# Performance work log

Hardware: AMD Instinct MI355X
Metric: run time of the kernel (lower is better)

Reference implementation:

```python
import jax, jax.numpy as jnp
import numpy as np
from jax import lax

# ---- module constants (match init_kwargs) ----
B, C, H, W = 8, 32, 128, 128
OUT = 32
RB = 1                      # refer_band
GB = (1, 1)                 # init_guard_band
GB_MAX = 3
PAD = GB[0] + RB            # replication pad on all 4 sides (=2)
KH = GB[0] + GB[1] + 2 * RB # kernel_size[0] = 4
KW = 4                      # kernel_size[1]
N = KH * KW                 # 16 ring sampling points
EPS = 1e-5


def _gen_prf():
    """Ring offsets (top,right,bottom,left blocks), matches _gen_prf_grid."""
    rb, gb = RB, GB
    h_prf = (rb + gb[0]) * 2 + 1
    w_prf = (rb + gb[1]) * 2 + 1
    xs = np.arange(-(rb + gb[0]), rb + gb[0] + 1)
    ys = np.arange(-(rb + gb[1]), rb + gb[1] + 1)
    X, Y = np.meshgrid(xs, ys, indexing='ij')
    def ring(A):
        t = A[0:rb, 0:w_prf - rb]
        r = A[0:h_prf - rb, w_prf - rb:w_prf]
        d = A[h_prf - rb:h_prf, rb:w_prf]
        l = A[rb:h_prf, 0:rb]
        return np.concatenate([t.ravel(), r.ravel(), d.ravel(), l.ravel()])
    return ring(X).astype(np.float32), ring(Y).astype(np.float32)

PRF_X, PRF_Y = _gen_prf()  # each (N,)


def _conv(x, w, b, pad, stride=(1, 1)):
    out = lax.conv_general_dilated(
        x, w, stride, [(pad[0], pad[0]), (pad[1], pad[1])],
        dimension_numbers=('NCHW', 'OIHW', 'NCHW'))
    return out + b[None, :, None, None]


def _bn(x, gamma, beta):
    # training-mode batchnorm (biased variance), matching torch default
    m = jnp.mean(x, (0, 2, 3), keepdims=True)
    v = jnp.var(x, (0, 2, 3), keepdims=True)
    return (x - m) * jax.lax.rsqrt(v + EPS) * gamma[None, :, None, None] + beta[None, :, None, None]


def _sample(x_flat, ix, iy, Wp, h, w):
    # x_flat: (B, C, Hp*Wp); ix, iy: (B, h, w, N) int -> (B, C, h, w, N)
    b = ix.shape[0]
    c = x_flat.shape[1]
    idx = (ix * Wp + iy).reshape(b, 1, -1)
    g = jnp.take_along_axis(x_flat, idx, axis=2)
    return g.reshape(b, c, h, w, N)


def _forward(x, w_vrt, b_vrt, g_vrt, be_vrt, w_hrz, b_hrz, g_hrz, be_hrz, w_pk, b_pk):
    b, c, h, w = x.shape
    x_pad = jnp.pad(x, ((0, 0), (0, 0), (PAD, PAD), (PAD, PAD)), mode='edge')
    Hp, Wp = x_pad.shape[2], x_pad.shape[3]
    x_flat = x_pad.reshape(b, c, Hp * Wp)

    # ---- BandEst: per-pixel guard-band widths in 4 directions (B,4,H,W) ----
    v = jax.nn.sigmoid(_bn(_conv(x, w_vrt, b_vrt, (GB_MAX, 0)), g_vrt, be_vrt)) * (GB_MAX - 1)
    hz = jax.nn.sigmoid(_bn(_conv(x, w_hrz, b_hrz, (0, GB_MAX)), g_hrz, be_hrz)) * (GB_MAX - 1)
    gb = jnp.concatenate([v, hz], axis=1)

    # ---- reference-cell sampling positions p = center + ring + learned move ----
    base_x = (jnp.arange(h, dtype=x.dtype) + PAD)[None, :, None, None]
    base_y = (jnp.arange(w, dtype=x.dtype) + PAD)[None, None, :, None]
    p_x = base_x + jnp.asarray(PRF_X)[None, None, None, :]  # (1,H,1,N)->bcast
    p_y = base_y + jnp.asarray(PRF_Y)[None, None, None, :]

    n4 = N // 4  # points per ring side (t,r,d,l ordering)
    def rep(g2):  # (B,H,W) -> (B,H,W,n4)
        return jnp.broadcast_to(g2[..., None], (b, h, w, n4))
    zeros = jnp.zeros((b, h, w, n4), x.dtype)
    move_x = jnp.concatenate([-rep(gb[:, 0]), zeros, rep(gb[:, 1]), zeros], -1)
    move_y = jnp.concatenate([zeros, rep(gb[:, 3]), zeros, -rep(gb[:, 2])], -1)
    p_x = p_x + move_x  # (B,H,W,N)
    p_y = p_y + move_y

    # ---- bilinear (two-corner) gather, mirrors torch q_lt/q_rb/g_lt/g_rb ----
    q_lt_x = jnp.floor(lax.stop_gradient(p_x))
    q_lt_y = jnp.floor(lax.stop_gradient(p_y))
    q_rb_x, q_rb_y = q_lt_x + 1, q_lt_y + 1
    q_lt_xi = jnp.clip(q_lt_x, 0, Hp - 1).astype(jnp.int32)
    q_lt_yi = jnp.clip(q_lt_y, 0, Wp - 1).astype(jnp.int32)
    q_rb_xi = jnp.clip(q_rb_x, 0, Hp - 1).astype(jnp.int32)
    q_rb_yi = jnp.clip(q_rb_y, 0, Wp - 1).astype(jnp.int32)
    p_x = jnp.clip(p_x, 0, Hp - 1)
    p_y = jnp.clip(p_y, 0, Wp - 1)

    g_lt = (1 + (q_lt_xi.astype(p_x.dtype) - p_x)) * (1 + (q_lt_yi.astype(p_y.dtype) - p_y))
    g_rb = (1 - (q_rb_xi.astype(p_x.dtype) - p_x)) * (1 - (q_rb_yi.astype(p_y.dtype) - p_y))

    x_q_lt = _sample(x_flat, q_lt_xi, q_lt_yi, Wp, h, w)  # (B,C,H,W,N)
    x_q_rb = _sample(x_flat, q_rb_xi, q_rb_yi, Wp, h, w)
    x_r = g_lt[:, None] * x_q_lt + g_rb[:, None] * x_q_rb

    # center value x_c equals x itself (center indices land in the interior)
    x_prf = x[:, :, :, :, None] - x_r  # (B,C,H,W,N)

    # ---- _reshape_x_prf: (B,C,H,W,N) -> (B,C,H*KH,W*KW) ----
    xk = x_prf.reshape(b, c, h, w, KH, KW).transpose(0, 1, 2, 4, 3, 5).reshape(b, c, h * KH, w * KW)

    # ---- peak conv: kernel = stride = (KH,KW), no padding ----
    return _conv(xk, w_pk, b_pk, (0, 0), stride=(KH, KW))


def setup_inputs() -> dict:
    key = jax.random.key(0)
    ks = jax.random.split(key, 8)
    s = 0.05
    return {
        'x': jax.random.normal(ks[0], (B, C, H, W), jnp.float32),
        'w_vrt': jax.random.normal(ks[1], (2, C, 2 * GB_MAX + 1, 1), jnp.float32) * s,
        'b_vrt': jax.random.normal(ks[2], (2,), jnp.float32) * s,
        'g_vrt': jnp.ones((2,), jnp.float32),
        'be_vrt': jnp.zeros((2,), jnp.float32),
        'w_hrz': jax.random.normal(ks[3], (2, C, 1, 2 * GB_MAX + 1), jnp.float32) * s,
        'b_hrz': jax.random.normal(ks[4], (2,), jnp.float32) * s,
        'g_hrz': jnp.ones((2,), jnp.float32),
        'be_hrz': jnp.zeros((2,), jnp.float32),
        'w_pk': jax.random.normal(ks[5], (OUT, C, KH, KW), jnp.float32) * s,
        'b_pk': jax.random.normal(ks[6], (OUT,), jnp.float32) * s,
    }


def reference(x, w_vrt, b_vrt, g_vrt, be_vrt, w_hrz, b_hrz, g_hrz, be_hrz, w_pk, b_pk):
    return _forward(x, w_vrt, b_vrt, g_vrt, be_vrt, w_hrz, b_hrz, g_hrz, be_hrz, w_pk, b_pk)
```

## Files before the change

kernel.cpp:

```cpp
#include <hip/hip_runtime.h>
#include <math.h>

#define BB 8
#define CCH 32
#define HH 128
#define WW 128
#define OUTC 32
#define NPIX (BB*HH*WW)
#define HWP 131

#define WS_XTB   0
#define WS_VO2   2097152
#define WS_HO2   (WS_VO2 + NPIX*2)
#define WS_PARTV (WS_HO2 + NPIX*2)
#define WS_PARTH (WS_PARTV + 2048*4)
#define WS_WKB   (WS_PARTH + 1024*4)

#define TILE_USH (12*40*5*8)

typedef __attribute__((ext_vector_type(8))) short short8;
typedef __attribute__((ext_vector_type(4))) float f32x4;

__device__ __forceinline__ unsigned short f2bf(float f) {
    unsigned u = __float_as_uint(f);
    unsigned r = (u + 0x7FFFu + ((u >> 16) & 1u)) >> 16;
    return (unsigned short)r;
}
__device__ __forceinline__ unsigned cvtpk(float lo, float hi) {
    unsigned r;
    asm("v_cvt_pk_bf16_f32 %0, %1, %2" : "=v"(r) : "v"(lo), "v"(hi));
    return r;
}
__device__ __forceinline__ float bflo(unsigned w) { return __uint_as_float(w << 16); }
__device__ __forceinline__ float bfhi(unsigned w) { return __uint_as_float(w & 0xFFFF0000u); }

__global__ __launch_bounds__(256) void k_fused1(const float* __restrict__ x,
        const float* __restrict__ w_vrt, const float* __restrict__ b_vrt,
        const float* __restrict__ w_hrz, const float* __restrict__ b_hrz,
        const float* __restrict__ w_pk, float* __restrict__ ws) {
    __shared__ unsigned sbuf[12288];
    int blk = blockIdx.x, t = threadIdx.x;
    if (blk < 256) {
        int jh = blk & 1, istr = (blk >> 1) & 15, b = blk >> 5;
        int i0 = istr * 8;
        int px = t & 63;
        int sub = __builtin_amdgcn_readfirstlane(t >> 6);
        int col = jh * 64 + px;
        unsigned* xp = sbuf;
        float* red_v = (float*)(sbuf + 8192);
        float vo[8][2];
        #pragma unroll
        for (int r = 0; r < 8; r++) { vo[r][0] = 0.f; vo[r][1] = 0.f; }
        float prev[8];
        for (int c8 = 0; c8 < 8; c8++) {
            int c = sub * 8 + c8;
            const float* basec = x + ((size_t)(b*CCH + c))*HH*WW;
            float xv[14];
            #pragma unroll
            for (int rr = 0; rr < 14; rr++) {
                int gr = i0 - 3 + rr;
                xv[rr] = ((unsigned)gr < (unsigned)HH) ? basec[(size_t)gr*WW + col] : 0.f;
            }
            #pragma unroll
            for (int r = 0; r < 8; r++) {
                #pragma unroll
                for (int k = 0; k < 7; k++) {
                    float wv0 = w_vrt[c*7 + k], wv1 = w_vrt[224 + c*7 + k];
                    vo[r][0] += wv0 * xv[r + k];
                    vo[r][1] += wv1 * xv[r + k];
                }
            }
            if ((c8 & 1) == 0) {
                #pragma unroll
                for (int r = 0; r < 8; r++) prev[r] = xv[3 + r];
            } else {
                #pragma unroll
                for (int r = 0; r < 8; r++)
                    xp[(r*64 + px)*16 + sub*4 + (c8 >> 1)] = cvtpk(prev[r], xv[3 + r]);
            }
        }
        #pragma unroll
        for (int r = 0; r < 8; r++) {
            red_v[((sub*64 + px)*8 + r)*2 + 0] = vo[r][0];
            red_v[((sub*64 + px)*8 + r)*2 + 1] = vo[r][1];
        }
        __syncthreads();
        float2* vo2 = (float2*)(ws + WS_VO2);
        #pragma unroll
        for (int h2 = 0; h2 < 2; h2++) {
            int r2 = sub * 2 + h2;
            float fv0 = red_v[((0*64 + px)*8 + r2)*2 + 0] + red_v[((1*64 + px)*8 + r2)*2 + 0]
                      + red_v[((2*64 + px)*8 + r2)*2 + 0] + red_v[((3*64 + px)*8 + r2)*2 + 0]
                      + b_vrt[0];
            float fv1 = red_v[((0*64 + px)*8 + r2)*2 + 1] + red_v[((1*64 + px)*8 + r2)*2 + 1]
                      + red_v[((2*64 + px)*8 + r2)*2 + 1] + red_v[((3*64 + px)*8 + r2)*2 + 1]
                      + b_vrt[1];
            int i = i0 + r2;
            vo2[(size_t)(b << 14) + i * WW + col] = make_float2(fv0, fv1);
            int cb = (b*HH + i)*2 + jh;
            float stv[4] = {fv0, fv1, fv0*fv0, fv1*fv1};
            #pragma unroll
            for (int u = 0; u < 4; u++) {
                float s = stv[u];
                for (int off = 32; off; off >>= 1) s += __shfl_down(s, off);
                if (px == 0) ws[WS_PARTV + cb*4 + u] = s;
            }
        }
        {
            uint4* xtb4 = (uint4*)(ws + WS_XTB);
            const uint4* xp4 = (const uint4*)xp;
            #pragma unroll
            for (int u = 0; u < 8; u++) {
                int e4 = u*256 + t;
                int rr = e4 >> 8, rem = e4 & 255, jj = rem >> 2, c4 = rem & 3;
                xtb4[(size_t)((b*HH + i0 + rr)*WW + jh*64 + jj)*4 + c4]
                    = xp4[(rr*64 + jj)*4 + c4];
            }
        }
    } else if (blk < 1280) {
        int e = blk - 256;
        int b = e >> 7, i = e & 127;
        int px2 = t & 63;
        int sub = __builtin_amdgcn_readfirstlane(t >> 6);
        float* red_h = (float*)sbuf;
        int cc[5]; bool mv[10];
        #pragma unroll
        for (int u = 0; u < 5; u++) {
            int c2 = 2*px2 - 4 + 2*u;
            cc[u] = min(max(c2, 0), WW - 2);
            mv[2*u]   = (unsigned)c2 < (unsigned)WW;
            mv[2*u+1] = (unsigned)(c2 + 1) < (unsigned)WW;
        }
        float h0A = 0.f, h1A = 0.f, h0B = 0.f, h1B = 0.f;
        for (int c8 = 0; c8 < 8; c8++) {
            int c = sub * 8 + c8;
            const float* rowb = x + ((size_t)(b*CCH + c)*HH + i)*WW;
            float lo[10];
            #pragma unroll
            for (int u = 0; u < 5; u++) {
                float2 v = *(const float2*)(rowb + cc[u]);
                lo[2*u]   = mv[2*u]   ? v.x : 0.f;
                lo[2*u+1] = mv[2*u+1] ? v.y : 0.f;
            }
            #pragma unroll
            for (int k = 0; k < 7; k++) {
                float wh0 = w_hrz[c*7 + k], wh1 = w_hrz[224 + c*7 + k];
                h0A += wh0 * lo[k+1]; h1A += wh1 * lo[k+1];
                h0B += wh0 * lo[k+2]; h1B += wh1 * lo[k+2];
            }
        }
        red_h[(sub*64 + px2)*4 + 0] = h0A;
        red_h[(sub*64 + px2)*4 + 1] = h0B;
        red_h[(sub*64 + px2)*4 + 2] = h1A;
        red_h[(sub*64 + px2)*4 + 3] = h1B;
        __syncthreads();
        if (sub == 0) {
            float fh0A = red_h[(0*64+px2)*4+0] + red_h[(1*64+px2)*4+0]
                       + red_h[(2*64+px2)*4+0] + red_h[(3*64+px2)*4+0] + b_hrz[0];
            float fh0B = red_h[(0*64+px2)*4+1] + red_h[(1*64+px2)*4+1]
                       + red_h[(2*64+px2)*4+1] + red_h[(3*64+px2)*4+1] + b_hrz[0];
            float fh1A = red_h[(0*64+px2)*4+2] + red_h[(1*64+px2)*4+2]
                       + red_h[(2*64+px2)*4+2] + red_h[(3*64+px2)*4+2] + b_hrz[1];
            float fh1B = red_h[(0*64+px2)*4+3] + red_h[(1*64+px2)*4+3]
                       + red_h[(2*64+px2)*4+3] + red_h[(3*64+px2)*4+3] + b_hrz[1];
            float2* ho2 = (float2*)(ws + WS_HO2);
            size_t pix = (size_t)(b << 14) + i * WW + 2*px2;
            *(float4*)(ho2 + pix) = make_float4(fh0A, fh1A, fh0B, fh1B);
            float stv[4] = {fh0A + fh0B, fh1A + fh1B,
                            fh0A*fh0A + fh0B*fh0B, fh1A*fh1A + fh1B*fh1B};
            #pragma unroll
            for (int u = 0; u < 4; u++) {
                float s = stv[u];
                for (int off = 32; off; off >>= 1) s += __shfl_down(s, off);
                if (px2 == 0) ws[WS_PARTH + e*4 + u] = s;
            }
        }
    } else {
        unsigned short* wkb = (unsigned short*)(ws + WS_WKB);
        int e = (blk - 1280) * 2048 + t;
        for (int u = 0; u < 8; u++, e += 256) {
            int o = e >> 9, n = (e >> 5) & 15, c = e & 31;
            wkb[o*512 + n*32 + c] = f2bf(w_pk[((o*32 + c) << 4) + n]);
        }
    }
}

__device__ __forceinline__ short8 sample_frag(const unsigned short* tile,
        const float* xc8, const float* gbv, float fi, float fj, int n,
        float prx, float pry, int i0, int j0, int quad) {
    float mx = 0.f, my = 0.f;
    if (n < 4)       mx = -gbv[0];
    else if (n < 8)  my =  gbv[3];
    else if (n < 12) mx =  gbv[1];
    else             my = -gbv[2];
    float px = fi + prx + mx;
    float py = fj + pry + my;
    float qlx = floorf(px), qly = floorf(py);
    int qlxi = min(max((int)qlx, 0), HWP);
    int qlyi = min(max((int)qly, 0), HWP);
    int qrxi = min(max((int)qlx + 1, 0), HWP);
    int qryi = min(max((int)qly + 1, 0), HWP);
    float pxc = fminf(fmaxf(px, 0.f), (float)HWP);
    float pyc = fminf(fmaxf(py, 0.f), (float)HWP);
    float glt = (1.f + ((float)qlxi - pxc)) * (1.f + ((float)qlyi - pyc));
    float grb = (1.f - ((float)qrxi - pxc)) * (1.f - ((float)qryi - pyc));
    float nglt = -glt, ngrb = -grb;
    int ltr = min(max(qlxi - 2, 0), HH - 1), ltc = min(max(qlyi - 2, 0), WW - 1);
    int rbr = min(max(qrxi - 2, 0), HH - 1), rbc = min(max(qryi - 2, 0), WW - 1);
    int lt_off = (ltr - i0 + 4)*1600 + (ltc - j0 + 4)*40 + quad*8;
    int rb_off = (rbr - i0 + 4)*1600 + (rbc - j0 + 4)*40 + quad*8;
    uint4 lw = *(const uint4*)(tile + lt_off);
    uint4 rw = *(const uint4*)(tile + rb_off);
    float d0 = fmaf(nglt, bflo(lw.x), fmaf(ngrb, bflo(rw.x), xc8[0]));
    float d1 = fmaf(nglt, bfhi(lw.x), fmaf(ngrb, bfhi(rw.x), xc8[1]));
    float d2 = fmaf(nglt, bflo(lw.y), fmaf(ngrb, bflo(rw.y), xc8[2]));
    float d3 = fmaf(nglt, bfhi(lw.y), fmaf(ngrb, bfhi(rw.y), xc8[3]));
    float d4 = fmaf(nglt, bflo(lw.z), fmaf(ngrb, bflo(rw.z), xc8[4]));
    float d5 = fmaf(nglt, bfhi(lw.z), fmaf(ngrb, bfhi(rw.z), xc8[5]));
    float d6 = fmaf(nglt, bflo(lw.w), fmaf(ngrb, bflo(rw.w), xc8[6]));
    float d7 = fmaf(nglt, bfhi(lw.w), fmaf(ngrb, bfhi(rw.w), xc8[7]));
    uint4 bw;
    bw.x = cvtpk(d0, d1); bw.y = cvtpk(d2, d3);
    bw.z = cvtpk(d4, d5); bw.w = cvtpk(d6, d7);
    return *(short8*)&bw;
}

__device__ __forceinline__ void frac_setup(float pm, float& ng, int& m) {
    float qf = floorf(pm);
    int qi = min(max((int)qf, 0), HWP);
    float pmc = fminf(fmaxf(pm, 0.f), (float)HWP);
    ng = pmc - (float)qi - 1.f;
    m = min(max(qi - 2, 0), HH - 1);
}
__device__ __forceinline__ short8 samp1(const unsigned short* tile,
        const float* xc8, float ng, int off) {
    uint4 lw = *(const uint4*)(tile + off);
    float d0 = fmaf(ng, bflo(lw.x), xc8[0]);
    float d1 = fmaf(ng, bfhi(lw.x), xc8[1]);
    float d2 = fmaf(ng, bflo(lw.y), xc8[2]);
    float d3 = fmaf(ng, bfhi(lw.y), xc8[3]);
    float d4 = fmaf(ng, bflo(lw.z), xc8[4]);
    float d5 = fmaf(ng, bfhi(lw.z), xc8[5]);
    float d6 = fmaf(ng, bflo(lw.w), xc8[6]);
    float d7 = fmaf(ng, bfhi(lw.w), xc8[7]);
    uint4 bw;
    bw.x = cvtpk(d0, d1); bw.y = cvtpk(d2, d3);
    bw.z = cvtpk(d4, d5); bw.w = cvtpk(d6, d7);
    return *(short8*)&bw;
}

__global__ __launch_bounds__(256, 4) void k_main(const float* __restrict__ ws,
        const float* __restrict__ x,
        const float* __restrict__ g_vrt, const float* __restrict__ be_vrt,
        const float* __restrict__ g_hrz, const float* __restrict__ be_hrz,
        const float* __restrict__ b_pk, float* __restrict__ out) {
    __shared__ unsigned short tile[TILE_USH];
    __shared__ float racc[32][8];
    __shared__ float bnab_s[8];
    const unsigned short* xtb = (const unsigned short*)(ws + WS_XTB);
    const unsigned short* wkb = (const unsigned short*)(ws + WS_WKB);
    const float* partv = ws + WS_PARTV;
    const float* parth = ws + WS_PARTH;
    const float prfx[16] = {-2,-2,-2,-2, -2,-1, 0, 1,  2, 2, 2, 2, -1, 0, 1, 2};
    const float prfy[16] = {-2,-1, 0, 1,  2, 2, 2, 2, -1, 0, 1, 2, -2,-2,-2,-2};
    const int ioffs[16]  = {-2,-1, 0, 1, -2,-1, 0, 1, -1, 0, 1, 2, -1, 0, 1, 2};

    int t = threadIdx.x;
    int blk = ((blockIdx.x & 7) << 7) | (blockIdx.x >> 3);
    int b = blk >> 7;
    int i0 = ((blk >> 2) & 31) * 4;
    int j0 = (blk & 3) * 32;

    for (int s = t; s < 12*40*4; s += 256) {
        int q = s & 3, cc = (s >> 2) % 40, r = (s >> 2) / 40;
        int gr = min(max(i0 - 4 + r, 0), HH - 1);
        int gc = min(max(j0 - 4 + cc, 0), WW - 1);
        uint4 v = *(const uint4*)(xtb + (((size_t)(b*HH + gr))*WW + gc)*CCH + q*8);
        *(uint4*)(tile + ((r*40 + cc)*5 + q)*8) = v;
    }
    {
        int s8 = t & 7, chunk = t >> 3;
        int col = (s8 & 1) + ((s8 >> 2) << 1);
        bool isv = ((s8 >> 1) & 1) == 0;
        float sum = 0.f;
        if (isv) {
            for (int m = 0; m < 64; m++)
                sum += partv[(size_t)(chunk*64 + m)*4 + col];
        } else {
            for (int m = 0; m < 32; m++)
                sum += parth[(size_t)(chunk*32 + m)*4 + col];
        }
        racc[chunk][s8] = sum;
    }
    __syncthreads();
    if (t < 8) {
        float tot = 0.f;
        #pragma unroll
        for (int c = 0; c < 32; c++) tot += racc[c][t];
        racc[0][t] = tot;
    }
    __syncthreads();
    if (t < 4) {
        const float cnt = (float)NPIX;
        float mean = racc[0][t] / cnt;
        float var  = racc[0][4 + t] / cnt - mean * mean;
        float gamma = (t < 2) ? g_vrt[t] : g_hrz[t - 2];
        float beta  = (t < 2) ? be_vrt[t] : be_hrz[t - 2];
        float a = gamma * rsqrtf(var + 1e-5f);
        bnab_s[t]     = a;
        bnab_s[4 + t] = beta - mean * a;
    }
    __syncthreads();

    int w = t >> 6, pl = t & 15, quad = (t >> 4) & 3;
    int ir = i0 + w;
    int pjA = j0 + pl, pjB = j0 + 16 + pl;
    int pixA = (b << 14) + ir * WW + pjA;
    int pixB = pixA + 16;
    int q8 = quad * 8;

    float xcA[8], xcB[8];
    {
        const float* xb = x + (size_t)b * CCH * HH * WW + (size_t)ir * WW;
        #pragma unroll
        for (int k = 0; k < 8; k++) {
            const float* p = xb + (size_t)(q8 + k) * (HH * WW);
            xcA[k] = p[pjA];
            xcB[k] = p[pjB];
        }
    }
    const float2* vo2 = (const float2*)(ws + WS_VO2);
    const float2* ho2 = (const float2*)(ws + WS_HO2);
    float2 vA = vo2[pixA], hA = ho2[pixA];
    float2 vB = vo2[pixB], hB = ho2[pixB];
    float gbvA[4], gbvB[4];
    gbvA[0] = 2.f / (1.f + expf(-(vA.x * bnab_s[0] + bnab_s[4])));
    gbvA[1] = 2.f / (1.f + expf(-(vA.y * bnab_s[1] + bnab_s[5])));
    gbvA[2] = 2.f / (1.f + expf(-(hA.x * bnab_s[2] + bnab_s[6])));
    gbvA[3] = 2.f / (1.f + expf(-(hA.y * bnab_s[3] + bnab_s[7])));
    gbvB[0] = 2.f / (1.f + expf(-(vB.x * bnab_s[0] + bnab_s[4])));
    gbvB[1] = 2.f / (1.f + expf(-(vB.y * bnab_s[1] + bnab_s[5])));
    gbvB[2] = 2.f / (1.f + expf(-(hB.x * bnab_s[2] + bnab_s[6])));
    gbvB[3] = 2.f / (1.f + expf(-(hB.y * bnab_s[3] + bnab_s[7])));

    f32x4 accA0 = {0.f,0.f,0.f,0.f}, accA1 = {0.f,0.f,0.f,0.f};
    f32x4 accB0 = {0.f,0.f,0.f,0.f}, accB1 = {0.f,0.f,0.f,0.f};
    float fi = (float)ir + 2.f;
    float fjA = (float)pjA + 2.f, fjB = (float)pjB + 2.f;

    short8 a0 = *(const short8*)(wkb + (size_t)pl * 512 + q8);
    short8 a1 = *(const short8*)(wkb + (size_t)(pl + 16) * 512 + q8);

    float ngA_ = 0.f, ngB_ = 0.f;
    int baseA_ = 0, baseB_ = 0;

    #pragma unroll
    for (int n = 0; n < 16; n++) {
        short8 na0 = a0, na1 = a1;
        if (n < 15) {
            na0 = *(const short8*)(wkb + (size_t)pl * 512 + (n+1)*32 + q8);
            na1 = *(const short8*)(wkb + (size_t)(pl + 16) * 512 + (n+1)*32 + q8);
        }
        if ((n & 3) == 0) {
            int g = n >> 2;
            float pmA, pmB;
            if (g == 0)      { pmA = (fi  - 2.f) - gbvA[0]; pmB = (fi  - 2.f) - gbvB[0]; }
            else if (g == 1) { pmA = (fjA + 2.f) + gbvA[3]; pmB = (fjB + 2.f) + gbvB[3]; }
            else if (g == 2) { pmA = (fi  + 2.f) + gbvA[1]; pmB = (fi  + 2.f) + gbvB[1]; }
            else             { pmA = (fjA - 2.f) - gbvA[2]; pmB = (fjB - 2.f) - gbvB[2]; }
            int mA, mB;
            frac_setup(pmA, ngA_, mA);
            frac_setup(pmB, ngB_, mB);
            if ((g & 1) == 0) {
                baseA_ = (mA - i0 + 4)*1600 + q8;
                baseB_ = (mB - i0 + 4)*1600 + q8;
            } else {
                baseA_ = (mA - j0 + 4)*40 + q8;
                baseB_ = (mB - j0 + 4)*40 + q8;
            }
        }
        short8 bfA, bfB;
        if (n == 11 || n == 15) {
            bfA = sample_frag(tile, xcA, gbvA, fi, fjA, n, prfx[n], prfy[n], i0, j0, quad);
            bfB = sample_frag(tile, xcB, gbvB, fi, fjB, n, prfx[n], prfy[n], i0, j0, quad);
        } else {
            int io = ioffs[n];
            int offA, offB;
            if (((n >> 2) & 1) == 0) {
                int cA = min(max(pjA + io, 0), WW - 1);
                int cB = min(max(pjB + io, 0), WW - 1);
                offA = baseA_ + (cA - j0 + 4)*40;
                offB = baseB_ + (cB - j0 + 4)*40;
            } else {
                int r  = min(max(ir + io, 0), HH - 1);
                int rt = (r - i0 + 4)*1600;
                offA = baseA_ + rt;
                offB = baseB_ + rt;
            }
            bfA = samp1(tile, xcA, ngA_, offA);
            bfB = samp1(tile, xcB, ngB_, offB);
        }
        accA0 = __builtin_amdgcn_mfma_f32_16x16x32_bf16(a0, bfA, accA0, 0, 0, 0);
        accA1 = __builtin_amdgcn_mfma_f32_16x16x32_bf16(a1, bfA, accA1, 0, 0, 0);
        accB0 = __builtin_amdgcn_mfma_f32_16x16x32_bf16(a0, bfB, accB0, 0, 0, 0);
        accB1 = __builtin_amdgcn_mfma_f32_16x16x32_bf16(a1, bfB, accB1, 0, 0, 0);
        a0 = na0; a1 = na1;
    }
    float* opA = out + (size_t)b * (OUTC*HH*WW) + ir * WW + pjA;
    float* opB = opA + 16;
    #pragma unroll
    for (int r = 0; r < 4; r++) {
        int o = quad*4 + r;
        float bo = b_pk[o], bo16 = b_pk[o + 16];
        opA[(size_t)o * (HH*WW)]        = accA0[r] + bo;
        opA[(size_t)(o + 16) * (HH*WW)] = accA1[r] + bo16;
        opB[(size_t)o * (HH*WW)]        = accB0[r] + bo;
        opB[(size_t)(o + 16) * (HH*WW)] = accB1[r] + bo16;
    }
}

extern "C" void kernel_launch(void* const* d_in, const int* in_sizes, int n_in,
                              void* d_out, int out_size, void* d_ws, size_t ws_size,
                              hipStream_t stream) {
    const float* x      = (const float*)d_in[0];
    const float* w_vrt  = (const float*)d_in[1];
    const float* b_vrt  = (const float*)d_in[2];
    const float* g_vrt  = (const float*)d_in[3];
    const float* be_vrt = (const float*)d_in[4];
    const float* w_hrz  = (const float*)d_in[5];
    const float* b_hrz  = (const float*)d_in[6];
    const float* g_hrz  = (const float*)d_in[7];
    const float* be_hrz = (const float*)d_in[8];
    const float* w_pk   = (const float*)d_in[9];
    const float* b_pk   = (const float*)d_in[10];
    float* ws  = (float*)d_ws;
    float* out = (float*)d_out;

    k_fused1<<<256 + 1024 + 8, 256, 0, stream>>>(x, w_vrt, b_vrt, w_hrz, b_hrz, w_pk, ws);
    k_main<<<1024, 256, 0, stream>>>(ws, x, g_vrt, be_vrt, g_hrz, be_hrz, b_pk, out);
}
```

Measured before the change: 128.3 us.

## Split vertical conv blocks finer and vectorize BN partial-stat reduction

The vertical-conv phase of the first kernel now uses 512 blocks of 32 columns with 8 channel groups, instead of 256 blocks of 64 columns with 4 groups. This doubles parallelism and cuts shared memory per block, and the reduction buffer gets a padded stride of 17 to avoid bank conflicts. In the main kernel, every block re-reduces the BN partial sums; this now uses coalesced float4 loads plus wave shuffles instead of strided scalar loops. The cost is a larger cross-block reduction and twice as many partial records to re-read in each main block.

```diff
diff --git a/kernel.cpp b/kernel.cpp
--- a/kernel.cpp
+++ b/kernel.cpp
@@ -13,7 +13,7 @@
 #define WS_VO2   2097152
 #define WS_HO2   (WS_VO2 + NPIX*2)
 #define WS_PARTV (WS_HO2 + NPIX*2)
-#define WS_PARTH (WS_PARTV + 2048*4)
+#define WS_PARTH (WS_PARTV + 4096*4)
 #define WS_WKB   (WS_PARTH + 1024*4)
 
 #define TILE_USH (12*40*5*8)
@@ -38,22 +38,22 @@
         const float* __restrict__ w_vrt, const float* __restrict__ b_vrt,
         const float* __restrict__ w_hrz, const float* __restrict__ b_hrz,
         const float* __restrict__ w_pk, float* __restrict__ ws) {
-    __shared__ unsigned sbuf[12288];
+    __shared__ unsigned sbuf[8448];
     int blk = blockIdx.x, t = threadIdx.x;
-    if (blk < 256) {
-        int jh = blk & 1, istr = (blk >> 1) & 15, b = blk >> 5;
+    if (blk < 512) {
+        int jq = blk & 3, istr = (blk >> 2) & 15, b = blk >> 6;
         int i0 = istr * 8;
-        int px = t & 63;
-        int sub = __builtin_amdgcn_readfirstlane(t >> 6);
-        int col = jh * 64 + px;
+        int px = t & 31;
+        int sub = t >> 5;
+        int col = jq * 32 + px;
         unsigned* xp = sbuf;
-        float* red_v = (float*)(sbuf + 8192);
+        float* red_v = (float*)(sbuf + 4096);
         float vo[8][2];
         #pragma unroll
         for (int r = 0; r < 8; r++) { vo[r][0] = 0.f; vo[r][1] = 0.f; }
         float prev[8];
-        for (int c8 = 0; c8 < 8; c8++) {
-            int c = sub * 8 + c8;
+        for (int c4 = 0; c4 < 4; c4++) {
+            int c = sub * 4 + c4;
             const float* basec = x + ((size_t)(b*CCH + c))*HH*WW;
             float xv[14];
             #pragma unroll
@@ -70,55 +70,55 @@
                     vo[r][1] += wv1 * xv[r + k];
                 }
             }
-            if ((c8 & 1) == 0) {
+            if ((c4 & 1) == 0) {
                 #pragma unroll
                 for (int r = 0; r < 8; r++) prev[r] = xv[3 + r];
             } else {
                 #pragma unroll
                 for (int r = 0; r < 8; r++)
-                    xp[(r*64 + px)*16 + sub*4 + (c8 >> 1)] = cvtpk(prev[r], xv[3 + r]);
+                    xp[(r*32 + px)*16 + sub*2 + (c4 >> 1)] = cvtpk(prev[r], xv[3 + r]);
             }
         }
         #pragma unroll
         for (int r = 0; r < 8; r++) {
-            red_v[((sub*64 + px)*8 + r)*2 + 0] = vo[r][0];
-            red_v[((sub*64 + px)*8 + r)*2 + 1] = vo[r][1];
+            red_v[(sub*32 + px)*17 + r*2 + 0] = vo[r][0];
+            red_v[(sub*32 + px)*17 + r*2 + 1] = vo[r][1];
         }
         __syncthreads();
-        float2* vo2 = (float2*)(ws + WS_VO2);
-        #pragma unroll
-        for (int h2 = 0; h2 < 2; h2++) {
-            int r2 = sub * 2 + h2;
-            float fv0 = red_v[((0*64 + px)*8 + r2)*2 + 0] + red_v[((1*64 + px)*8 + r2)*2 + 0]
-                      + red_v[((2*64 + px)*8 + r2)*2 + 0] + red_v[((3*64 + px)*8 + r2)*2 + 0]
-                      + b_vrt[0];
-            float fv1 = red_v[((0*64 + px)*8 + r2)*2 + 1] + red_v[((1*64 + px)*8 + r2)*2 + 1]
-                      + red_v[((2*64 + px)*8 + r2)*2 + 1] + red_v[((3*64 + px)*8 + r2)*2 + 1]
-                      + b_vrt[1];
-            int i = i0 + r2;
-            vo2[(size_t)(b << 14) + i * WW + col] = make_float2(fv0, fv1);
-            int cb = (b*HH + i)*2 + jh;
+        {
+            int rr = t >> 5, pxc = t & 31;
+            float s0 = red_v[(0*32 + pxc)*17 + rr*2 + 0];
+            float s1 = red_v[(0*32 + pxc)*17 + rr*2 + 1];
+            #pragma unroll
+            for (int sb = 1; sb < 8; sb++) {
+                s0 += red_v[(sb*32 + pxc)*17 + rr*2 + 0];
+                s1 += red_v[(sb*32 + pxc)*17 + rr*2 + 1];
+            }
+            float fv0 = s0 + b_vrt[0], fv1 = s1 + b_vrt[1];
+            int i = i0 + rr;
+            float2* vo2 = (float2*)(ws + WS_VO2);
+            vo2[(size_t)(b << 14) + i * WW + jq*32 + pxc] = make_float2(fv0, fv1);
+            int cb4 = (b*HH + i)*4 + jq;
             float stv[4] = {fv0, fv1, fv0*fv0, fv1*fv1};
             #pragma unroll
             for (int u = 0; u < 4; u++) {
                 float s = stv[u];
-                for (int off = 32; off; off >>= 1) s += __shfl_down(s, off);
-                if (px == 0) ws[WS_PARTV + cb*4 + u] = s;
+                for (int off = 16; off; off >>= 1) s += __shfl_down(s, off);
+                if (pxc == 0) ws[WS_PARTV + cb4*4 + u] = s;
             }
         }
         {
             uint4* xtb4 = (uint4*)(ws + WS_XTB);
             const uint4* xp4 = (const uint4*)xp;
             #pragma unroll
-            for (int u = 0; u < 8; u++) {
+            for (int u = 0; u < 4; u++) {
                 int e4 = u*256 + t;
-                int rr = e4 >> 8, rem = e4 & 255, jj = rem >> 2, c4 = rem & 3;
-                xtb4[(size_t)((b*HH + i0 + rr)*WW + jh*64 + jj)*4 + c4]
-                    = xp4[(rr*64 + jj)*4 + c4];
-            }
-        }
-    } else if (blk < 1280) {
-        int e = blk - 256;
+                int rr2 = e4 >> 7, rem = e4 & 127, jj = rem >> 2, c4i = rem & 3;
+                xtb4[(size_t)((b*HH + i0 + rr2)*WW + jq*32 + jj)*4 + c4i] = xp4[e4];
+            }
+        }
+    } else if (blk < 1536) {
+        int e = blk - 512;
         int b = e >> 7, i = e & 127;
         int px2 = t & 63;
         int sub = __builtin_amdgcn_readfirstlane(t >> 6);
@@ -177,7 +177,7 @@
         }
     } else {
         unsigned short* wkb = (unsigned short*)(ws + WS_WKB);
-        int e = (blk - 1280) * 2048 + t;
+        int e = (blk - 1536) * 2048 + t;
         for (int u = 0; u < 8; u++, e += 256) {
             int o = e >> 9, n = (e >> 5) & 15, c = e & 31;
             wkb[o*512 + n*32 + c] = f2bf(w_pk[((o*32 + c) << 4) + n]);
@@ -255,12 +255,10 @@
         const float* __restrict__ g_hrz, const float* __restrict__ be_hrz,
         const float* __restrict__ b_pk, float* __restrict__ out) {
     __shared__ unsigned short tile[TILE_USH];
-    __shared__ float racc[32][8];
+    __shared__ float racc[4][8];
     __shared__ float bnab_s[8];
     const unsigned short* xtb = (const unsigned short*)(ws + WS_XTB);
     const unsigned short* wkb = (const unsigned short*)(ws + WS_WKB);
-    const float* partv = ws + WS_PARTV;
-    const float* parth = ws + WS_PARTH;
     const float prfx[16] = {-2,-2,-2,-2, -2,-1, 0, 1,  2, 2, 2, 2, -1, 0, 1, 2};
     const float prfy[16] = {-2,-1, 0, 1,  2, 2, 2, 2, -1, 0, 1, 2, -2,-2,-2,-2};
     const int ioffs[16]  = {-2,-1, 0, 1, -2,-1, 0, 1, -1, 0, 1, 2, -1, 0, 1, 2};
@@ -279,26 +277,35 @@
         *(uint4*)(tile + ((r*40 + cc)*5 + q)*8) = v;
     }
     {
-        int s8 = t & 7, chunk = t >> 3;
-        int col = (s8 & 1) + ((s8 >> 2) << 1);
-        bool isv = ((s8 >> 1) & 1) == 0;
-        float sum = 0.f;
-        if (isv) {
-            for (int m = 0; m < 64; m++)
-                sum += partv[(size_t)(chunk*64 + m)*4 + col];
-        } else {
-            for (int m = 0; m < 32; m++)
-                sum += parth[(size_t)(chunk*32 + m)*4 + col];
-        }
-        racc[chunk][s8] = sum;
+        const float4* pv4 = (const float4*)(ws + WS_PARTV);
+        const float4* ph4 = (const float4*)(ws + WS_PARTH);
+        float4 sv = make_float4(0.f,0.f,0.f,0.f), sh = make_float4(0.f,0.f,0.f,0.f);
+        #pragma unroll 4
+        for (int m = 0; m < 16; m++) {
+            float4 v = pv4[t + 256*m];
+            sv.x += v.x; sv.y += v.y; sv.z += v.z; sv.w += v.w;
+        }
+        #pragma unroll 4
+        for (int m = 0; m < 4; m++) {
+            float4 v = ph4[t + 256*m];
+            sh.x += v.x; sh.y += v.y; sh.z += v.z; sh.w += v.w;
+        }
+        #pragma unroll
+        for (int off = 32; off; off >>= 1) {
+            sv.x += __shfl_down(sv.x, off); sv.y += __shfl_down(sv.y, off);
+            sv.z += __shfl_down(sv.z, off); sv.w += __shfl_down(sv.w, off);
+            sh.x += __shfl_down(sh.x, off); sh.y += __shfl_down(sh.y, off);
+            sh.z += __shfl_down(sh.z, off); sh.w += __shfl_down(sh.w, off);
+        }
+        if ((t & 63) == 0) {
+            int wv = t >> 6;
+            racc[wv][0] = sv.x; racc[wv][1] = sv.y; racc[wv][2] = sh.x; racc[wv][3] = sh.y;
+            racc[wv][4] = sv.z; racc[wv][5] = sv.w; racc[wv][6] = sh.z; racc[wv][7] = sh.w;
+        }
     }
     __syncthreads();
-    if (t < 8) {
-        float tot = 0.f;
-        #pragma unroll
-        for (int c = 0; c < 32; c++) tot += racc[c][t];
-        racc[0][t] = tot;
-    }
+    if (t < 8)
+        racc[0][t] = racc[0][t] + racc[1][t] + racc[2][t] + racc[3][t];
     __syncthreads();
     if (t < 4) {
         const float cnt = (float)NPIX;
@@ -436,6 +443,6 @@
     float* ws  = (float*)d_ws;
     float* out = (float*)d_out;
 
-    k_fused1<<<256 + 1024 + 8, 256, 0, stream>>>(x, w_vrt, b_vrt, w_hrz, b_hrz, w_pk, ws);
+    k_fused1<<<512 + 1024 + 8, 256, 0, stream>>>(x, w_vrt, b_vrt, w_hrz, b_hrz, w_pk, ws);
     k_main<<<1024, 256, 0, stream>>>(ws, x, g_vrt, be_vrt, g_hrz, be_hrz, b_pk, out);
 }
```

Result: faster. 124.6 us, median of 2 (-2.9%).
